# Kernel tuning notes

Hardware: AMD Instinct MI355X
Metric: run time of the kernel (lower is better)

## Reference

```python
import jax, jax.numpy as jnp
import numpy as np


def setup_inputs() -> dict:
    key = jax.random.key(0)
    k1, k2 = jax.random.split(key)
    B, C, H, W = 16, 256, 96, 96
    x1 = jax.random.normal(k1, (B, C, H, W), dtype=jnp.float32)
    x2 = jax.random.normal(k2, (B, C, H, W), dtype=jnp.float32)
    return {"x1": x1, "x2": x2, "k": 1, "d": 4, "s1": 1, "s2": 1}


def reference(x1, x2, k, d, s1, s2):
    """FlowNet-style correlation cost volume (k=1 pointwise patch).

    out[b, i, y, x] = (1/(k*k*C)) * sum_c x1[b,c,y,x] * x2_pad[b,c,y+dy_i,x+dx_i]
    for displacements (dy, dx) in [-d, d] with stride s2 (x2 zero-padded by d).
    Output strided by s1 over spatial dims. Output channels = (2*d//s2 + 1)**2.
    """
    assert k == 1, "reference specialized to k=1 (pointwise correlation)"
    B, C, H, W = x1.shape
    norm = 1.0 / (k * k * C)
    # zero-pad x2 by max displacement d on each spatial side
    x2p = jnp.pad(x2, ((0, 0), (0, 0), (d, d), (d, d)))
    offsets = list(range(-d, d + 1, s2))  # displacement grid (fixed, small)
    outs = []
    for dy in offsets:
        for dx in offsets:
            shifted = x2p[:, :, d + dy:d + dy + H, d + dx:d + dx + W]  # [B,C,H,W]
            outs.append(jnp.einsum('bchw,bchw->bhw', x1, shifted) * norm)
    out = jnp.stack(outs, axis=1)  # [B, D*D, H, W]
    return out[:, :, ::s1, ::s1]
```

## Files before the change

### kernel.cpp

```cpp
#include <hip/hip_runtime.h>


namespace {
constexpr int Bsz = 16, Cch = 256, Hh = 96, Ww = 96;
constexpr int Dd = 4, NDisp = 9;
constexpr int TH = 4;
constexpr int PX = 8;
constexpr int NSTRIP = Ww / PX;
constexpr int CC = 4;
constexpr int X2ROWS = TH + 2 * Dd;
constexpr int NT = TH * NDisp * NSTRIP;
constexpr int HW = Hh * Ww;

constexpr int CHUNK = 12;
constexpr int X1CH  = Ww / 8;
constexpr int X1RP  = X1CH * CHUNK;
constexpr int X1_LDS = CC * TH * X1RP;
constexpr int X2COLS = 104;
constexpr int X2CH  = X2COLS / 8;
constexpr int X2RP  = X2CH * CHUNK;
constexpr int X2_LDS = CC * X2ROWS * X2RP;
constexpr int X2_GROUPS = X2COLS / 4;
constexpr int X1_F4 = CC * TH * Ww / 4;
constexpr int X2_F4 = CC * X2ROWS * X2_GROUPS;
constexpr int N_ITEMS = X1_F4 + X2_F4;
}

__global__ __launch_bounds__(NT, 2)
void corr81(const float* __restrict__ x1, const float* __restrict__ x2,
            float* __restrict__ out) {
  __shared__ __align__(16) float lds[X1_LDS + X2_LDS + 4];

  const int t = threadIdx.x;
  const int y0 = blockIdx.x * TH;
  const int b  = blockIdx.y;

  const int r   = t / (NDisp * NSTRIP);
  const int rem = t % (NDisp * NSTRIP);
  const int dyi = rem / NSTRIP;
  const int s   = rem % NSTRIP;
  const int x0  = s * PX;

  const float* __restrict__ x1b = x1 + (size_t)b * Cch * HW;
  const float* __restrict__ x2b = x2 + (size_t)b * Cch * HW;

  const float* gp[4];
  int  loff[4];
  bool zero[4];
#pragma unroll
  for (int j = 0; j < 4; ++j) {
    int i = t + j * NT;
    if (i >= N_ITEMS) {
      gp[j] = x1b; loff[j] = X1_LDS + X2_LDS; zero[j] = true;
    } else if (i < X1_F4) {
      int c    = i / (TH * Ww / 4);
      int q    = i % (TH * Ww / 4);
      int grow = q / (Ww / 4);
      int col  = (q % (Ww / 4)) * 4;
      gp[j]   = x1b + c * HW + (size_t)(y0 + grow) * Ww + col;
      loff[j] = c * (TH * X1RP) + grow * X1RP + (col >> 3) * CHUNK + (col & 7);
      zero[j] = false;
    } else {
      int m  = i - X1_F4;
      int c  = m / (X2ROWS * X2_GROUPS);
      int m2 = m % (X2ROWS * X2_GROUPS);
      int ry = m2 / X2_GROUPS;
      int g  = m2 % X2_GROUPS;
      int pc = g * 4;
      int gy = y0 + ry - Dd;
      bool z = (gy < 0) | (gy >= Hh) | (g == 0) | (g == X2_GROUPS - 1);
      gp[j]   = z ? x2b : (x2b + c * HW + gy * Ww + (pc - 4));
      loff[j] = X1_LDS + c * (X2ROWS * X2RP) + ry * X2RP
              + (pc >> 3) * CHUNK + (pc & 7);
      zero[j] = z;
    }
  }

  float acc[NDisp][PX];
#pragma unroll
  for (int i = 0; i < NDisp; ++i)
#pragma unroll
    for (int j = 0; j < PX; ++j) acc[i][j] = 0.f;

  const float* ap0 = lds + r * X1RP + s * CHUNK;
  const float* bp0 = lds + X1_LDS + (r + dyi) * X2RP + s * CHUNK;

  float4 v[4];
#pragma unroll
  for (int j = 0; j < 4; ++j)
    v[j] = zero[j] ? make_float4(0.f, 0.f, 0.f, 0.f) : *(const float4*)gp[j];

  for (int c0 = 0; c0 < Cch; c0 += CC) {
    __syncthreads();
#pragma unroll
    for (int j = 0; j < 4; ++j)
      *(float4*)(lds + loff[j]) = v[j];
    __syncthreads();
    if (c0 + CC < Cch) {
#pragma unroll
      for (int j = 0; j < 4; ++j) {
        gp[j] += CC * HW;
        v[j] = zero[j] ? make_float4(0.f, 0.f, 0.f, 0.f) : *(const float4*)gp[j];
      }
    }
#pragma unroll
    for (int cc = 0; cc < CC; ++cc) {
      const float* ap = ap0 + cc * (TH * X1RP);
      float a[PX];
      *(float4*)(a)     = *(const float4*)(ap);
      *(float4*)(a + 4) = *(const float4*)(ap + 4);
      const float* bp = bp0 + cc * (X2ROWS * X2RP);
      float bb[PX + 2 * Dd];
      *(float4*)(bb)      = *(const float4*)(bp);
      *(float4*)(bb + 4)  = *(const float4*)(bp + 4);
      *(float4*)(bb + 8)  = *(const float4*)(bp + CHUNK);
      *(float4*)(bb + 12) = *(const float4*)(bp + CHUNK + 4);
#pragma unroll
      for (int dx = 0; dx < NDisp; ++dx)
#pragma unroll
        for (int px = 0; px < PX; ++px)
          acc[dx][px] += a[px] * bb[px + dx];
    }
  }

  const float nrm = 1.0f / (float)Cch;
  float* ob = out + ((size_t)b * (NDisp * NDisp) + (size_t)dyi * NDisp) * HW
                  + (size_t)(y0 + r) * Ww + x0;
#pragma unroll
  for (int dx = 0; dx < NDisp; ++dx) {
    float4 w0, w1;
    w0.x = acc[dx][0] * nrm; w0.y = acc[dx][1] * nrm;
    w0.z = acc[dx][2] * nrm; w0.w = acc[dx][3] * nrm;
    w1.x = acc[dx][4] * nrm; w1.y = acc[dx][5] * nrm;
    w1.z = acc[dx][6] * nrm; w1.w = acc[dx][7] * nrm;
    *(float4*)(ob + (size_t)dx * HW)     = w0;
    *(float4*)(ob + (size_t)dx * HW + 4) = w1;
  }
}

extern "C" void kernel_launch(void* const* d_in, const int* in_sizes, int n_in,
                              void* d_out, int out_size, void* d_ws, size_t ws_size,
                              hipStream_t stream) {
  const float* x1 = (const float*)d_in[0];
  const float* x2 = (const float*)d_in[1];
  float* out = (float*)d_out;
  dim3 grid(Hh / TH, Bsz);
  dim3 block(NT);
  hipLaunchKernelGGL(corr81, grid, block, 0, stream, x1, x2, out);
}
```

Before: 413.3 us.

## Split channels across blocks with atomic reduction and double-buffered LDS

Splits the channel reduction across two blocks per tile (grid z dimension), combining partial sums with atomicAdd into a pre-zeroed output. It also double-buffers the LDS staging so each stage needs one barrier, and remaps threads so displacement row varies fastest. This aims to raise block count and overlap loads with compute, at the cost of a memset, doubled LDS, and scalar atomic output traffic.

```diff
diff --git a/kernel.cpp b/kernel.cpp
--- a/kernel.cpp
+++ b/kernel.cpp
@@ -11,38 +11,42 @@
 constexpr int X2ROWS = TH + 2 * Dd;
 constexpr int NT = TH * NDisp * NSTRIP;
 constexpr int HW = Hh * Ww;
+constexpr int CSPLIT = 2;
+constexpr int CPB = Cch / CSPLIT;
+constexpr int NSTAGE = CPB / CC;
 
 constexpr int CHUNK = 12;
-constexpr int X1CH  = Ww / 8;
-constexpr int X1RP  = X1CH * CHUNK;
+constexpr int X1RP  = (Ww / 8) * CHUNK;
 constexpr int X1_LDS = CC * TH * X1RP;
 constexpr int X2COLS = 104;
-constexpr int X2CH  = X2COLS / 8;
-constexpr int X2RP  = X2CH * CHUNK;
+constexpr int X2RP  = (X2COLS / 8) * CHUNK;
 constexpr int X2_LDS = CC * X2ROWS * X2RP;
 constexpr int X2_GROUPS = X2COLS / 4;
 constexpr int X1_F4 = CC * TH * Ww / 4;
 constexpr int X2_F4 = CC * X2ROWS * X2_GROUPS;
 constexpr int N_ITEMS = X1_F4 + X2_F4;
+constexpr int BUF  = X1_LDS + X2_LDS;
+constexpr int BUFP = BUF + 4;
 }
 
 __global__ __launch_bounds__(NT, 2)
 void corr81(const float* __restrict__ x1, const float* __restrict__ x2,
             float* __restrict__ out) {
-  __shared__ __align__(16) float lds[X1_LDS + X2_LDS + 4];
+  __shared__ __align__(16) float lds[2 * BUFP];
 
-  const int t = threadIdx.x;
+  const int t  = threadIdx.x;
   const int y0 = blockIdx.x * TH;
   const int b  = blockIdx.y;
+  const int cb = blockIdx.z * CPB;
 
   const int r   = t / (NDisp * NSTRIP);
   const int rem = t % (NDisp * NSTRIP);
-  const int dyi = rem / NSTRIP;
-  const int s   = rem % NSTRIP;
+  const int s   = rem / NDisp;
+  const int dyi = rem % NDisp;
   const int x0  = s * PX;
 
-  const float* __restrict__ x1b = x1 + (size_t)b * Cch * HW;
-  const float* __restrict__ x2b = x2 + (size_t)b * Cch * HW;
+  const float* __restrict__ x1b = x1 + ((size_t)b * Cch + cb) * HW;
+  const float* __restrict__ x2b = x2 + ((size_t)b * Cch + cb) * HW;
 
   const float* gp[4];
   int  loff[4];
@@ -51,7 +55,7 @@
   for (int j = 0; j < 4; ++j) {
     int i = t + j * NT;
     if (i >= N_ITEMS) {
-      gp[j] = x1b; loff[j] = X1_LDS + X2_LDS; zero[j] = true;
+      gp[j] = x1b; loff[j] = BUF; zero[j] = true;
     } else if (i < X1_F4) {
       int c    = i / (TH * Ww / 4);
       int q    = i % (TH * Ww / 4);
@@ -89,27 +93,27 @@
 #pragma unroll
   for (int j = 0; j < 4; ++j)
     v[j] = zero[j] ? make_float4(0.f, 0.f, 0.f, 0.f) : *(const float4*)gp[j];
+#pragma unroll
+  for (int j = 0; j < 4; ++j)
+    *(float4*)(lds + loff[j]) = v[j];
+#pragma unroll
+  for (int j = 0; j < 4; ++j) {
+    gp[j] += CC * HW;
+    v[j] = zero[j] ? make_float4(0.f, 0.f, 0.f, 0.f) : *(const float4*)gp[j];
+  }
+  __syncthreads();
 
-  for (int c0 = 0; c0 < Cch; c0 += CC) {
-    __syncthreads();
-#pragma unroll
-    for (int j = 0; j < 4; ++j)
-      *(float4*)(lds + loff[j]) = v[j];
-    __syncthreads();
-    if (c0 + CC < Cch) {
-#pragma unroll
-      for (int j = 0; j < 4; ++j) {
-        gp[j] += CC * HW;
-        v[j] = zero[j] ? make_float4(0.f, 0.f, 0.f, 0.f) : *(const float4*)gp[j];
-      }
-    }
+#pragma unroll 2
+  for (int k = 0; k < NSTAGE; ++k) {
+    const float* ap_b = ap0 + (k & 1) * BUFP;
+    const float* bp_b = bp0 + (k & 1) * BUFP;
 #pragma unroll
     for (int cc = 0; cc < CC; ++cc) {
-      const float* ap = ap0 + cc * (TH * X1RP);
+      const float* ap = ap_b + cc * (TH * X1RP);
       float a[PX];
       *(float4*)(a)     = *(const float4*)(ap);
       *(float4*)(a + 4) = *(const float4*)(ap + 4);
-      const float* bp = bp0 + cc * (X2ROWS * X2RP);
+      const float* bp = bp_b + cc * (X2ROWS * X2RP);
       float bb[PX + 2 * Dd];
       *(float4*)(bb)      = *(const float4*)(bp);
       *(float4*)(bb + 4)  = *(const float4*)(bp + 4);
@@ -121,21 +125,30 @@
         for (int px = 0; px < PX; ++px)
           acc[dx][px] += a[px] * bb[px + dx];
     }
+    if (k + 1 < NSTAGE) {
+      float* wb = lds + ((k + 1) & 1) * BUFP;
+#pragma unroll
+      for (int j = 0; j < 4; ++j)
+        *(float4*)(wb + loff[j]) = v[j];
+      if (k + 2 < NSTAGE) {
+#pragma unroll
+        for (int j = 0; j < 4; ++j) {
+          gp[j] += CC * HW;
+          v[j] = zero[j] ? make_float4(0.f, 0.f, 0.f, 0.f) : *(const float4*)gp[j];
+        }
+      }
+    }
+    __syncthreads();
   }
 
   const float nrm = 1.0f / (float)Cch;
   float* ob = out + ((size_t)b * (NDisp * NDisp) + (size_t)dyi * NDisp) * HW
                   + (size_t)(y0 + r) * Ww + x0;
 #pragma unroll
-  for (int dx = 0; dx < NDisp; ++dx) {
-    float4 w0, w1;
-    w0.x = acc[dx][0] * nrm; w0.y = acc[dx][1] * nrm;
-    w0.z = acc[dx][2] * nrm; w0.w = acc[dx][3] * nrm;
-    w1.x = acc[dx][4] * nrm; w1.y = acc[dx][5] * nrm;
-    w1.z = acc[dx][6] * nrm; w1.w = acc[dx][7] * nrm;
-    *(float4*)(ob + (size_t)dx * HW)     = w0;
-    *(float4*)(ob + (size_t)dx * HW + 4) = w1;
-  }
+  for (int dx = 0; dx < NDisp; ++dx)
+#pragma unroll
+    for (int px = 0; px < PX; ++px)
+      atomicAdd(ob + (size_t)dx * HW + px, acc[dx][px] * nrm);
 }
 
 extern "C" void kernel_launch(void* const* d_in, const int* in_sizes, int n_in,
@@ -144,7 +157,8 @@
   const float* x1 = (const float*)d_in[0];
   const float* x2 = (const float*)d_in[1];
   float* out = (float*)d_out;
-  dim3 grid(Hh / TH, Bsz);
+  hipMemsetAsync(d_out, 0, (size_t)out_size, stream);
+  dim3 grid(Hh / TH, Bsz, CSPLIT);
   dim3 block(NT);
   hipLaunchKernelGGL(corr81, grid, block, 0, stream, x1, x2, out);
 }
```

New measurement: 1.612 ms. +290.1%, slower.
